# Optimization experiments

Measured on AMD Instinct MI355X. Metric: run time of the kernel, lower is better.

The kernel has to match this reference:

```python
import jax, jax.numpy as jnp
import numpy as np

N, E = 100000, 400000
ATOM_DIM, HIDDEN, LAYERS, HEADS = 74, 256, 3, 4
OUT = HIDDEN // HEADS


def setup_inputs() -> dict:
    key = jax.random.key(0)
    ks = jax.random.split(key, 12)
    s = 1.0 / np.sqrt(HIDDEN)
    return {
        'atom_feat': jax.random.normal(ks[0], (N, ATOM_DIM), jnp.float32),
        'src': jax.random.randint(ks[1], (E,), 0, N, jnp.int32),
        'dst': jax.random.randint(ks[2], (E,), 0, N, jnp.int32),
        'W_in': jax.random.normal(ks[3], (ATOM_DIM, HIDDEN), jnp.float32) / np.sqrt(ATOM_DIM),
        'b_in': jnp.zeros((HIDDEN,), jnp.float32),
        'W_src': jax.random.normal(ks[4], (LAYERS, HIDDEN, HIDDEN), jnp.float32) * s,
        'b_src': jnp.zeros((LAYERS, HIDDEN), jnp.float32),
        'W_dst': jax.random.normal(ks[5], (LAYERS, HIDDEN, HIDDEN), jnp.float32) * s,
        'b_dst': jnp.zeros((LAYERS, HIDDEN), jnp.float32),
        'attn': jax.random.normal(ks[6], (LAYERS, HEADS, OUT), jnp.float32) * s,
        'bias': jnp.zeros((LAYERS, HIDDEN), jnp.float32),
    }


def _gatv2_layer(h, src, dst, Ws, bs, Wd, bd, a, b_out):
    # h: [N, HIDDEN]; fc_src / fc_dst projections reshaped to [N, HEADS, OUT]
    fs = (h @ Ws + bs).reshape(N, HEADS, OUT)
    fd = (h @ Wd + bd).reshape(N, HEADS, OUT)
    # GATv2: e_ij = a . leaky_relu(Ws h_i + Wd h_j) per head  -> [E, HEADS]
    e = jax.nn.leaky_relu(fs[src] + fd[dst], negative_slope=0.2)
    logits = jnp.einsum('ehd,hd->eh', e, a)
    # segment softmax over incoming edges of each dst node
    m = jax.ops.segment_max(logits, dst, num_segments=N)      # [N, HEADS]
    ex = jnp.exp(logits - m[dst])
    denom = jax.ops.segment_sum(ex, dst, num_segments=N)      # [N, HEADS]
    alpha = ex / denom[dst]                                   # [E, HEADS]
    # weighted scatter-aggregate of source features -> [N, HEADS, OUT]
    msg = alpha[:, :, None] * fs[src]
    rst = jax.ops.segment_sum(msg, dst, num_segments=N)
    # flatten(1) + per-layer output bias
    return rst.reshape(N, HIDDEN) + b_out


def reference(atom_feat, src, dst, W_in, b_in, W_src, b_src, W_dst, b_dst, attn, bias):
    h = atom_feat @ W_in + b_in
    for l in range(LAYERS):
        h = _gatv2_layer(h, src, dst, W_src[l], b_src[l], W_dst[l], b_dst[l], attn[l], bias[l])
    return h  # [N, HIDDEN]; per-molecule list is just slicing of this matrix
```

## Files before the change

### kernel.cpp

```cpp
#include <hip/hip_runtime.h>
#include <hip/hip_fp16.h>

#define HID   256
#define NHEAD 4
#define DOUT  64
#define ADIM  74
#define KPAD_IN 96
#define LAYERS 3

typedef _Float16 half8 __attribute__((ext_vector_type(8)));
typedef _Float16 half4 __attribute__((ext_vector_type(4)));
typedef _Float16 half2v __attribute__((ext_vector_type(2)));
typedef float f32x4 __attribute__((ext_vector_type(4)));

__device__ __forceinline__ void gload16(const void* g, void* l) {
  __builtin_amdgcn_global_load_lds((const __attribute__((address_space(1))) void*)g,
                                   (__attribute__((address_space(3))) void*)l, 16, 0, 0);
}

__global__ void k_prep(const float* __restrict__ Ws, const float* __restrict__ Wd,
                       const float* __restrict__ Win,
                       _Float16* __restrict__ WT, _Float16* __restrict__ WTin) {
  int l = blockIdx.y;
  int id = blockIdx.x * 256 + threadIdx.x;
  if (l < LAYERS) {
    if (id >= 512 * HID) return;
    int n = id >> 8, k = id & 255;
    const float* W = (n < HID) ? (Ws + (size_t)l * HID * HID)
                               : (Wd + (size_t)l * HID * HID);
    int nn = (n < HID) ? n : (n - HID);
    WT[(size_t)l * 512 * HID + id] = (_Float16)W[k * HID + nn];
  } else {
    if (id >= HID * KPAD_IN) return;
    int n = id / KPAD_IN, k = id % KPAD_IN;
    WTin[id] = (_Float16)((k < ADIM) ? Win[k * HID + n] : 0.f);
  }
}

__device__ __forceinline__ void gemm_epilogue2(
    f32x4 acc[4][4], char* smem, int t, int lane, int wm, int wn,
    int row0, int col0, int M,
    const float* bias0, const float* bias1,
    _Float16* outS, _Float16* outD)
{
  const float* bp = (col0 < HID) ? (bias0 + col0) : (bias1 + (col0 - HID));
  _Float16*    op = (col0 < HID) ? (outS + col0) : (outD + (col0 - HID));
  _Float16 (*C)[136] = (_Float16(*)[136])smem;
  #pragma unroll
  for (int half = 0; half < 2; ++half) {
    __syncthreads();
    if (wm == half) {
      #pragma unroll
      for (int i = 0; i < 4; ++i) {
        #pragma unroll
        for (int j = 0; j < 4; ++j) {
          int lc = wn * 64 + j * 16 + (lane & 15);
          float bv = bp[lc];
          #pragma unroll
          for (int r = 0; r < 4; ++r) {
            int lr = i * 16 + (lane >> 4) * 4 + r;
            C[lr][lc] = (_Float16)(acc[i][j][r] + bv);
          }
        }
      }
    }
    __syncthreads();
    int lr = t >> 2, seg = t & 3;
    int grow = row0 + half * 64 + lr;
    if (grow < M) {
      const _Float16* sp = &C[lr][seg * 32];
      _Float16* dp = op + (size_t)grow * HID + seg * 32;
      #pragma unroll
      for (int q = 0; q < 4; ++q)
        *(uint4*)(dp + q * 8) = *(const uint4*)(sp + q * 8);
    }
  }
}

__global__ __launch_bounds__(256, 4)
void k_gemm_h(const _Float16* __restrict__ A, int M,
              const _Float16* __restrict__ B,
              const float* __restrict__ bias0, const float* __restrict__ bias1,
              _Float16* __restrict__ outS, _Float16* __restrict__ outD)
{
  __shared__ __align__(16) char smem[32768];
  const int t = threadIdx.x, lane = t & 63, wid = t >> 6;
  const int wm = wid >> 1, wn = wid & 1;
  const int nwg = gridDim.x, id = blockIdx.x;
  const int qc = nwg >> 3, rc = nwg & 7, xcd = id & 7, idx = id >> 3;
  const int swz = (xcd < rc ? xcd * (qc + 1) : rc * (qc + 1) + (xcd - rc) * qc) + idx;
  const int col0 = (swz & 3) * 128, row0 = (swz >> 2) * 128;

  f32x4 acc[4][4];
  #pragma unroll
  for (int i = 0; i < 4; ++i)
    #pragma unroll
    for (int j = 0; j < 4; ++j)
      acc[i][j] = (f32x4){0.f, 0.f, 0.f, 0.f};

  auto stage = [&](int kt, int buf) {
    const int kb = kt * 32;
    char* Ab = smem + buf * 16384;
    char* Bb = Ab + 8192;
    #pragma unroll
    for (int q = 0; q < 2; ++q) {
      int ci = wid * 2 + q;
      int lr = lane >> 2;
      int r = ci * 16 + lr;
      int slot = (lane & 3) ^ ((lr >> 1) & 3);
      int grow = row0 + r; grow = grow < M ? grow : (M - 1);
      gload16(A + (size_t)grow * HID + kb + slot * 8, Ab + ci * 1024);
      gload16(B + (size_t)(col0 + r) * HID + kb + slot * 8, Bb + ci * 1024);
    }
  };

  stage(0, 0);
  const int slot_off = (((lane >> 4) ^ ((lane >> 1) & 3)) << 4);
  const int ar0 = (wm * 64 + (lane & 15)) * 64 + slot_off;
  const int br0 = (wn * 64 + (lane & 15)) * 64 + slot_off;

  #pragma unroll
  for (int kt = 0; kt < 8; ++kt) {
    if (kt < 7) stage(kt + 1, (kt + 1) & 1);
    if (kt < 7) asm volatile("s_waitcnt vmcnt(4)" ::: "memory");
    else        asm volatile("s_waitcnt vmcnt(0)" ::: "memory");
    __builtin_amdgcn_s_barrier();
    __builtin_amdgcn_sched_barrier(0);
    const char* Ab = smem + (kt & 1) * 16384;
    const char* Bb = Ab + 8192;
    half8 af[4], bf[4];
    #pragma unroll
    for (int i = 0; i < 4; ++i) af[i] = *(const half8*)(Ab + ar0 + i * 1024);
    #pragma unroll
    for (int j = 0; j < 4; ++j) bf[j] = *(const half8*)(Bb + br0 + j * 1024);
    __builtin_amdgcn_s_setprio(1);
    #pragma unroll
    for (int i = 0; i < 4; ++i)
      #pragma unroll
      for (int j = 0; j < 4; ++j)
        acc[i][j] = __builtin_amdgcn_mfma_f32_16x16x32_f16(af[i], bf[j], acc[i][j], 0, 0, 0);
    __builtin_amdgcn_s_setprio(0);
    asm volatile("s_waitcnt lgkmcnt(0)" ::: "memory");
    __builtin_amdgcn_sched_barrier(0);
    __builtin_amdgcn_s_barrier();
    __builtin_amdgcn_sched_barrier(0);
  }
  gemm_epilogue2(acc, smem, t, lane, wm, wn, row0, col0, M, bias0, bias1, outS, outD);
}

__global__ __launch_bounds__(256)
void k_gemm_f(const float* __restrict__ A, int M,
              const _Float16* __restrict__ B,
              const float* __restrict__ bias0,
              _Float16* __restrict__ outS)
{
  __shared__ __align__(16) char smem[17408];
  const int t = threadIdx.x, lane = t & 63, wid = t >> 6;
  const int wm = wid >> 1, wn = wid & 1;
  const int nwg = gridDim.x, id = blockIdx.x;
  const int qc = nwg >> 3, rc = nwg & 7, xcd = id & 7, idx = id >> 3;
  const int swz = (xcd < rc ? xcd * (qc + 1) : rc * (qc + 1) + (xcd - rc) * qc) + idx;
  const int col0 = (swz & 1) * 128, row0 = (swz >> 1) * 128;
  char* Ab = smem;
  char* Bb = smem + 8192;

  f32x4 acc[4][4];
  #pragma unroll
  for (int i = 0; i < 4; ++i)
    #pragma unroll
    for (int j = 0; j < 4; ++j)
      acc[i][j] = (f32x4){0.f, 0.f, 0.f, 0.f};

  const int slot_off = (((lane >> 4) ^ ((lane >> 1) & 3)) << 4);
  const int ar0 = (wm * 64 + (lane & 15)) * 64 + slot_off;
  const int br0 = (wn * 64 + (lane & 15)) * 64 + slot_off;

  for (int kt = 0; kt < 3; ++kt) {
    const int kb = kt * 32;
    #pragma unroll
    for (int it = 0; it < 4; ++it) {
      int idx2 = t + it * 256;
      int r = idx2 >> 3, c4 = idx2 & 7;
      int gr = row0 + r;
      int k0 = kb + c4 * 4;
      float x0 = 0.f, x1 = 0.f, x2 = 0.f, x3 = 0.f;
      if (gr < M) {
        const float* ap = A + (size_t)gr * ADIM;
        if (k0 + 0 < ADIM) x0 = ap[k0 + 0];
        if (k0 + 1 < ADIM) x1 = ap[k0 + 1];
        if (k0 + 2 < ADIM) x2 = ap[k0 + 2];
        if (k0 + 3 < ADIM) x3 = ap[k0 + 3];
      }
      half4 hv = {(_Float16)x0, (_Float16)x1, (_Float16)x2, (_Float16)x3};
      int off = r * 64 + ((((c4 >> 1) ^ ((r >> 1) & 3)) << 4)) + (c4 & 1) * 8;
      *(half4*)(Ab + off) = hv;
    }
    #pragma unroll
    for (int q = 0; q < 2; ++q) {
      int ci = wid * 2 + q;
      int lr = lane >> 2;
      int r = ci * 16 + lr;
      int slot = (lane & 3) ^ ((lr >> 1) & 3);
      gload16(B + (size_t)(col0 + r) * KPAD_IN + kb + slot * 8, Bb + ci * 1024);
    }
    __syncthreads();
    half8 af[4], bf[4];
    #pragma unroll
    for (int i = 0; i < 4; ++i) af[i] = *(const half8*)(Ab + ar0 + i * 1024);
    #pragma unroll
    for (int j = 0; j < 4; ++j) bf[j] = *(const half8*)(Bb + br0 + j * 1024);
    #pragma unroll
    for (int i = 0; i < 4; ++i)
      #pragma unroll
      for (int j = 0; j < 4; ++j)
        acc[i][j] = __builtin_amdgcn_mfma_f32_16x16x32_f16(af[i], bf[j], acc[i][j], 0, 0, 0);
    __syncthreads();
  }
  gemm_epilogue2(acc, smem, t, lane, wm, wn, row0, col0, M, bias0, bias0, outS, outS);
}

__global__ __launch_bounds__(256)
void k_fused(const int* __restrict__ offs, const int* __restrict__ esrc,
             const int* __restrict__ perm,
             const _Float16* __restrict__ fs, const _Float16* __restrict__ fd,
             const float* __restrict__ attn, const float* __restrict__ bias,
             _Float16* __restrict__ hhalf, float* __restrict__ hfloat, int N)
{
  int gid = blockIdx.x * 8 + (threadIdx.x >> 5);
  if (gid >= N) return;
  int n = perm[gid];
  int sub = threadIdx.x & 31;
  int h = sub >> 3;
  int j0 = sub * 8;
  half8 fdv = *(const half8*)&fd[(size_t)n * HID + j0];
  float4 av0 = *(const float4*)&attn[h * DOUT + (sub & 7) * 8];
  float4 av1 = *(const float4*)&attn[h * DOUT + (sub & 7) * 8 + 4];
  float4 bv0 = *(const float4*)&bias[j0];
  float4 bv1 = *(const float4*)&bias[j0 + 4];
  half2v avh[4];
  avh[0] = (half2v){(_Float16)av0.x, (_Float16)av0.y};
  avh[1] = (half2v){(_Float16)av0.z, (_Float16)av0.w};
  avh[2] = (half2v){(_Float16)av1.x, (_Float16)av1.y};
  avh[3] = (half2v){(_Float16)av1.z, (_Float16)av1.w};
  half2v fd2[4];
  #pragma unroll
  for (int q = 0; q < 4; ++q) fd2[q] = (half2v){fdv[2 * q], fdv[2 * q + 1]};
  const half2v c02 = {(_Float16)0.2f, (_Float16)0.2f};
  float bvf[8] = {bv0.x, bv0.y, bv0.z, bv0.w, bv1.x, bv1.y, bv1.z, bv1.w};

  int t0 = offs[n], t1 = offs[n + 1];
  float m = -1e30f, ssum = 0.f;
  float a[8];
  #pragma unroll
  for (int q = 0; q < 8; ++q) a[q] = 0.f;

  half8 fE[4];
  #pragma unroll
  for (int k = 0; k < 4; ++k) {
    fE[k] = (half8){};
    if (t0 + k < t1) fE[k] = *(const half8*)&fs[(size_t)esrc[t0 + k] * HID + j0];
  }

  for (int tt = t0; tt < t1; tt += 4) {
    half8 fc[4];
    #pragma unroll
    for (int k = 0; k < 4; ++k) fc[k] = fE[k];
    #pragma unroll
    for (int k = 0; k < 4; ++k) {
      fE[k] = (half8){};
      if (tt + 4 + k < t1) fE[k] = *(const half8*)&fs[(size_t)esrc[tt + 4 + k] * HID + j0];
    }
    float p[4];
    #pragma unroll
    for (int k = 0; k < 4; ++k) {
      float acc = 0.f;
      #pragma unroll
      for (int q = 0; q < 4; ++q) {
        half2v xf = {fc[k][2 * q], fc[k][2 * q + 1]};
        half2v x = xf + fd2[q];
        half2v l = __builtin_elementwise_max(x, x * c02);
        acc = __builtin_amdgcn_fdot2(l, avh[q], acc, false);
      }
      p[k] = (tt + k < t1) ? acc : -1e30f;
    }
    #pragma unroll
    for (int k = 0; k < 4; ++k) {
      p[k] += __shfl_xor(p[k], 1);
      p[k] += __shfl_xor(p[k], 2);
      p[k] += __shfl_xor(p[k], 4);
    }
    float mx = fmaxf(fmaxf(fmaxf(p[0], p[1]), fmaxf(p[2], p[3])), m);
    float sc = __expf(m - mx);
    float w0 = __expf(p[0] - mx);
    float w1 = __expf(p[1] - mx);
    float w2 = __expf(p[2] - mx);
    float w3 = __expf(p[3] - mx);
    ssum = ssum * sc + w0 + w1 + w2 + w3;
    #pragma unroll
    for (int q = 0; q < 8; ++q) {
      float v = a[q] * sc;
      v += w0 * (float)fc[0][q];
      v += w1 * (float)fc[1][q];
      v += w2 * (float)fc[2][q];
      v += w3 * (float)fc[3][q];
      a[q] = v;
    }
    m = mx;
  }
  float inv = (t1 > t0) ? 1.0f / ssum : 0.f;
  float o[8];
  #pragma unroll
  for (int q = 0; q < 8; ++q) o[q] = a[q] * inv + bvf[q];
  if (hhalf) {
    half8 hv;
    #pragma unroll
    for (int q = 0; q < 8; ++q) hv[q] = (_Float16)o[q];
    *(half8*)&hhalf[(size_t)n * HID + j0] = hv;
  }
  if (hfloat) {
    float4 v0 = {o[0], o[1], o[2], o[3]};
    float4 v1 = {o[4], o[5], o[6], o[7]};
    *(float4*)&hfloat[(size_t)n * HID + j0] = v0;
    *(float4*)&hfloat[(size_t)n * HID + j0 + 4] = v1;
  }
}

__global__ void k_count(const int* __restrict__ dst, int* __restrict__ counts, int E) {
  int i = blockIdx.x * 256 + threadIdx.x;
  if (i < E) atomicAdd(&counts[dst[i]], 1);
}
__global__ __launch_bounds__(1024)
void k_scan1(const int* __restrict__ counts, int* __restrict__ offs,
             int* __restrict__ bsums, int* __restrict__ dhist, int N)
{
  __shared__ int sd[1024];
  __shared__ int hh[64];
  int t = threadIdx.x, i = blockIdx.x * 1024 + t;
  if (t < 64) hh[t] = 0;
  int x = (i < N) ? counts[i] : 0;
  sd[t] = x;
  __syncthreads();
  if (i < N) atomicAdd(&hh[x < 63 ? x : 63], 1);
  for (int off = 1; off < 1024; off <<= 1) {
    int v = (t >= off) ? sd[t - off] : 0;
    __syncthreads();
    sd[t] += v;
    __syncthreads();
  }
  if (i < N) offs[i] = sd[t] - x;
  if (t == 0) bsums[blockIdx.x] = sd[1023];
  __syncthreads();
  if (t < 64 && hh[t] > 0) atomicAdd(&dhist[t], hh[t]);
}
__global__ void k_scan2(const int* __restrict__ bsums, int* __restrict__ boffs,
                        int* __restrict__ offs, int nb, int N,
                        const int* __restrict__ dhist, int* __restrict__ dcur)
{
  int t = threadIdx.x;
  int x = dhist[t];
  int sum = x;
  for (int off = 1; off < 64; off <<= 1) {
    int v = __shfl_up(sum, off);
    if (t >= off) sum += v;
  }
  dcur[t] = sum - x;
  if (t == 0) {
    int run = 0;
    for (int b = 0; b < nb; ++b) { boffs[b] = run; run += bsums[b]; }
    offs[N] = run;
  }
}
__global__ __launch_bounds__(1024)
void k_scan3(const int* __restrict__ boffs, int* __restrict__ offs,
             int* __restrict__ cursor, int N)
{
  int i = blockIdx.x * 1024 + threadIdx.x;
  if (i < N) {
    int v = offs[i] + boffs[blockIdx.x];
    offs[i] = v;
    cursor[i] = v;
  }
}
__global__ void k_scatter(const int* __restrict__ src, const int* __restrict__ dst,
                          int* __restrict__ cursor, int* __restrict__ esrc, int E)
{
  int i = blockIdx.x * 256 + threadIdx.x;
  if (i < E) {
    int pos = atomicAdd(&cursor[dst[i]], 1);
    esrc[pos] = src[i];
  }
}
__global__ __launch_bounds__(256)
void k_deg_scatter(const int* __restrict__ counts, int* __restrict__ dcur,
                   int* __restrict__ perm, int N)
{
  __shared__ int hist[64];
  __shared__ int base[64];
  int t = threadIdx.x;
  int i = blockIdx.x * 256 + t;
  if (t < 64) hist[t] = 0;
  __syncthreads();
  int d = 0, lrank = 0;
  if (i < N) {
    d = counts[i]; d = d < 63 ? d : 63;
    lrank = atomicAdd(&hist[d], 1);
  }
  __syncthreads();
  if (t < 64 && hist[t] > 0) base[t] = atomicAdd(&dcur[t], hist[t]);
  __syncthreads();
  if (i < N) perm[base[d] + lrank] = i;
}

extern "C" void kernel_launch(void* const* d_in, const int* in_sizes, int n_in,
                              void* d_out, int out_size, void* d_ws, size_t ws_size,
                              hipStream_t stream)
{
  const float* atom  = (const float*)d_in[0];
  const int*   src   = (const int*)d_in[1];
  const int*   dst   = (const int*)d_in[2];
  const float* W_in  = (const float*)d_in[3];
  const float* b_in  = (const float*)d_in[4];
  const float* W_src = (const float*)d_in[5];
  const float* b_src = (const float*)d_in[6];
  const float* W_dst = (const float*)d_in[7];
  const float* b_dst = (const float*)d_in[8];
  const float* attn  = (const float*)d_in[9];
  const float* bias  = (const float*)d_in[10];

  const int N = in_sizes[0] / ADIM;
  const int E = in_sizes[1];
  _Float16* h_half = (_Float16*)d_out;
  float*    h_out  = (float*)d_out;

  char* w = (char*)d_ws;
  size_t off = 0;
  auto carve = [&](size_t bytes) {
    void* p = w + off;
    off = (off + bytes + 255) & ~(size_t)255;
    return p;
  };
  _Float16* fs    = (_Float16*)carve((size_t)N * HID * 2);
  _Float16* fd    = (_Float16*)carve((size_t)N * HID * 2);
  _Float16* WT    = (_Float16*)carve((size_t)LAYERS * 512 * HID * 2);
  _Float16* WTin  = (_Float16*)carve((size_t)HID * KPAD_IN * 2);
  int*      counts= (int*)carve((size_t)(N + 64) * 4);
  int*      offs  = (int*)carve((size_t)(N + 1) * 4);
  int*      cursor= (int*)carve((size_t)N * 4);
  int*      esrc  = (int*)carve((size_t)E * 4);
  int*      perm  = (int*)carve((size_t)N * 4);
  int*      dcur  = (int*)carve((size_t)64 * 4);
  int*      bsums = (int*)carve((size_t)1024 * 4);
  int*      boffs = (int*)carve((size_t)1024 * 4);
  int*      dhist = counts + N;
  (void)ws_size; (void)n_in; (void)out_size;

  const int nb = (N + 1023) / 1024;
  const int gmx = (N + 127) / 128;

  hipMemsetAsync(counts, 0, (size_t)(N + 64) * 4, stream);
  k_count<<<(E + 255) / 256, 256, 0, stream>>>(dst, counts, E);
  k_scan1<<<nb, 1024, 0, stream>>>(counts, offs, bsums, dhist, N);
  k_scan2<<<1, 64, 0, stream>>>(bsums, boffs, offs, nb, N, dhist, dcur);
  k_scan3<<<nb, 1024, 0, stream>>>(boffs, offs, cursor, N);
  k_scatter<<<(E + 255) / 256, 256, 0, stream>>>(src, dst, cursor, esrc, E);
  k_deg_scatter<<<(N + 255) / 256, 256, 0, stream>>>(counts, dcur, perm, N);

  k_prep<<<dim3(512, LAYERS + 1), 256, 0, stream>>>(W_src, W_dst, W_in, WT, WTin);
  k_gemm_f<<<2 * gmx, 256, 0, stream>>>(atom, N, WTin, b_in, h_half);

  for (int l = 0; l < LAYERS; ++l) {
    k_gemm_h<<<4 * gmx, 256, 0, stream>>>(h_half, N, WT + (size_t)l * 512 * HID,
                                          b_src + (size_t)l * HID,
                                          b_dst + (size_t)l * HID, fs, fd);
    const bool last = (l == LAYERS - 1);
    k_fused<<<(N + 7) / 8, 256, 0, stream>>>(offs, esrc, perm, fs, fd,
                                             attn + (size_t)l * NHEAD * DOUT,
                                             bias + (size_t)l * HID,
                                             last ? nullptr : h_half,
                                             last ? h_out : nullptr, N);
  }
}
```

Baseline: 458.4 us.

## Process two destination nodes per 32-lane group with interleaved edge loops

```diff
diff --git a/kernel.cpp b/kernel.cpp
--- a/kernel.cpp
+++ b/kernel.cpp
@@ -10,7 +10,6 @@
 
 typedef _Float16 half8 __attribute__((ext_vector_type(8)));
 typedef _Float16 half4 __attribute__((ext_vector_type(4)));
-typedef _Float16 half2v __attribute__((ext_vector_type(2)));
 typedef float f32x4 __attribute__((ext_vector_type(4)));
 
 __device__ __forceinline__ void gload16(const void* g, void* l) {
@@ -226,102 +225,132 @@
              const float* __restrict__ attn, const float* __restrict__ bias,
              _Float16* __restrict__ hhalf, float* __restrict__ hfloat, int N)
 {
-  int gid = blockIdx.x * 8 + (threadIdx.x >> 5);
-  if (gid >= N) return;
-  int n = perm[gid];
+  int grp = blockIdx.x * 8 + (threadIdx.x >> 5);
+  int g0 = grp * 2;
+  if (g0 >= N) return;
+  const bool has1 = (g0 + 1) < N;
+  int n0 = perm[g0];
+  int n1 = has1 ? perm[g0 + 1] : n0;
   int sub = threadIdx.x & 31;
   int h = sub >> 3;
   int j0 = sub * 8;
-  half8 fdv = *(const half8*)&fd[(size_t)n * HID + j0];
+
   float4 av0 = *(const float4*)&attn[h * DOUT + (sub & 7) * 8];
   float4 av1 = *(const float4*)&attn[h * DOUT + (sub & 7) * 8 + 4];
   float4 bv0 = *(const float4*)&bias[j0];
   float4 bv1 = *(const float4*)&bias[j0 + 4];
-  half2v avh[4];
-  avh[0] = (half2v){(_Float16)av0.x, (_Float16)av0.y};
-  avh[1] = (half2v){(_Float16)av0.z, (_Float16)av0.w};
-  avh[2] = (half2v){(_Float16)av1.x, (_Float16)av1.y};
-  avh[3] = (half2v){(_Float16)av1.z, (_Float16)av1.w};
-  half2v fd2[4];
-  #pragma unroll
-  for (int q = 0; q < 4; ++q) fd2[q] = (half2v){fdv[2 * q], fdv[2 * q + 1]};
-  const half2v c02 = {(_Float16)0.2f, (_Float16)0.2f};
+  float avf[8] = {av0.x, av0.y, av0.z, av0.w, av1.x, av1.y, av1.z, av1.w};
   float bvf[8] = {bv0.x, bv0.y, bv0.z, bv0.w, bv1.x, bv1.y, bv1.z, bv1.w};
 
-  int t0 = offs[n], t1 = offs[n + 1];
-  float m = -1e30f, ssum = 0.f;
-  float a[8];
-  #pragma unroll
-  for (int q = 0; q < 8; ++q) a[q] = 0.f;
-
-  half8 fE[4];
-  #pragma unroll
-  for (int k = 0; k < 4; ++k) {
-    fE[k] = (half8){};
-    if (t0 + k < t1) fE[k] = *(const half8*)&fs[(size_t)esrc[t0 + k] * HID + j0];
-  }
-
-  for (int tt = t0; tt < t1; tt += 4) {
-    half8 fc[4];
-    #pragma unroll
-    for (int k = 0; k < 4; ++k) fc[k] = fE[k];
-    #pragma unroll
-    for (int k = 0; k < 4; ++k) {
-      fE[k] = (half8){};
-      if (tt + 4 + k < t1) fE[k] = *(const half8*)&fs[(size_t)esrc[tt + 4 + k] * HID + j0];
-    }
-    float p[4];
-    #pragma unroll
-    for (int k = 0; k < 4; ++k) {
-      float acc = 0.f;
-      #pragma unroll
-      for (int q = 0; q < 4; ++q) {
-        half2v xf = {fc[k][2 * q], fc[k][2 * q + 1]};
-        half2v x = xf + fd2[q];
-        half2v l = __builtin_elementwise_max(x, x * c02);
-        acc = __builtin_amdgcn_fdot2(l, avh[q], acc, false);
-      }
-      p[k] = (tt + k < t1) ? acc : -1e30f;
-    }
-    #pragma unroll
-    for (int k = 0; k < 4; ++k) {
-      p[k] += __shfl_xor(p[k], 1);
-      p[k] += __shfl_xor(p[k], 2);
-      p[k] += __shfl_xor(p[k], 4);
-    }
-    float mx = fmaxf(fmaxf(fmaxf(p[0], p[1]), fmaxf(p[2], p[3])), m);
-    float sc = __expf(m - mx);
-    float w0 = __expf(p[0] - mx);
-    float w1 = __expf(p[1] - mx);
-    float w2 = __expf(p[2] - mx);
-    float w3 = __expf(p[3] - mx);
-    ssum = ssum * sc + w0 + w1 + w2 + w3;
+  half8 fdh0 = *(const half8*)&fd[(size_t)n0 * HID + j0];
+  half8 fdh1 = *(const half8*)&fd[(size_t)n1 * HID + j0];
+  float fd0[8], fd1[8];
+  #pragma unroll
+  for (int q = 0; q < 8; ++q) { fd0[q] = (float)fdh0[q]; fd1[q] = (float)fdh1[q]; }
+
+  int t00 = offs[n0], t01 = offs[n0 + 1];
+  int t10 = has1 ? offs[n1] : 0;
+  int t11 = has1 ? offs[n1 + 1] : 0;
+
+  float m0 = -1e30f, s0 = 0.f, m1 = -1e30f, s1 = 0.f;
+  float a0[8], a1[8];
+  #pragma unroll
+  for (int q = 0; q < 8; ++q) { a0[q] = 0.f; a1[q] = 0.f; }
+
+  half8 pA0 = {}, pB0 = {}, pA1 = {}, pB1 = {};
+  if (t00 < t01)     pA0 = *(const half8*)&fs[(size_t)esrc[t00] * HID + j0];
+  if (t00 + 1 < t01) pB0 = *(const half8*)&fs[(size_t)esrc[t00 + 1] * HID + j0];
+  if (t10 < t11)     pA1 = *(const half8*)&fs[(size_t)esrc[t10] * HID + j0];
+  if (t10 + 1 < t11) pB1 = *(const half8*)&fs[(size_t)esrc[t10 + 1] * HID + j0];
+
+  int tt0 = t00, tt1 = t10;
+  while (tt0 < t01 || tt1 < t11) {
+    const bool vA0 = tt0 < t01, vB0 = tt0 + 1 < t01;
+    const bool vA1 = tt1 < t11, vB1 = tt1 + 1 < t11;
+    half8 fA0 = pA0, fB0 = pB0, fA1 = pA1, fB1 = pB1;
+    pA0 = (half8){}; pB0 = (half8){}; pA1 = (half8){}; pB1 = (half8){};
+    if (tt0 + 2 < t01) pA0 = *(const half8*)&fs[(size_t)esrc[tt0 + 2] * HID + j0];
+    if (tt0 + 3 < t01) pB0 = *(const half8*)&fs[(size_t)esrc[tt0 + 3] * HID + j0];
+    if (tt1 + 2 < t11) pA1 = *(const half8*)&fs[(size_t)esrc[tt1 + 2] * HID + j0];
+    if (tt1 + 3 < t11) pB1 = *(const half8*)&fs[(size_t)esrc[tt1 + 3] * HID + j0];
+
+    float fa0[8], fb0[8], fa1[8], fb1[8];
     #pragma unroll
     for (int q = 0; q < 8; ++q) {
-      float v = a[q] * sc;
-      v += w0 * (float)fc[0][q];
-      v += w1 * (float)fc[1][q];
-      v += w2 * (float)fc[2][q];
-      v += w3 * (float)fc[3][q];
-      a[q] = v;
-    }
-    m = mx;
-  }
-  float inv = (t1 > t0) ? 1.0f / ssum : 0.f;
-  float o[8];
-  #pragma unroll
-  for (int q = 0; q < 8; ++q) o[q] = a[q] * inv + bvf[q];
+      fa0[q] = (float)fA0[q]; fb0[q] = (float)fB0[q];
+      fa1[q] = (float)fA1[q]; fb1[q] = (float)fB1[q];
+    }
+    float qa0 = 0.f, qb0 = 0.f, qa1 = 0.f, qb1 = 0.f;
+    #pragma unroll
+    for (int q = 0; q < 8; ++q) {
+      float x;
+      x = fa0[q] + fd0[q]; x = x > 0.f ? x : 0.2f * x; qa0 += x * avf[q];
+      x = fb0[q] + fd0[q]; x = x > 0.f ? x : 0.2f * x; qb0 += x * avf[q];
+      x = fa1[q] + fd1[q]; x = x > 0.f ? x : 0.2f * x; qa1 += x * avf[q];
+      x = fb1[q] + fd1[q]; x = x > 0.f ? x : 0.2f * x; qb1 += x * avf[q];
+    }
+    qa0 += __shfl_xor(qa0, 1); qb0 += __shfl_xor(qb0, 1);
+    qa1 += __shfl_xor(qa1, 1); qb1 += __shfl_xor(qb1, 1);
+    qa0 += __shfl_xor(qa0, 2); qb0 += __shfl_xor(qb0, 2);
+    qa1 += __shfl_xor(qa1, 2); qb1 += __shfl_xor(qb1, 2);
+    qa0 += __shfl_xor(qa0, 4); qb0 += __shfl_xor(qb0, 4);
+    qa1 += __shfl_xor(qa1, 4); qb1 += __shfl_xor(qb1, 4);
+    qa0 = vA0 ? qa0 : -1e30f;
+    qb0 = vB0 ? qb0 : -1e30f;
+    qa1 = vA1 ? qa1 : -1e30f;
+    qb1 = vB1 ? qb1 : -1e30f;
+    float mx0 = fmaxf(fmaxf(qa0, qb0), m0);
+    float sc0 = __expf(m0 - mx0);
+    float wa0 = __expf(qa0 - mx0);
+    float wb0 = __expf(qb0 - mx0);
+    float mx1 = fmaxf(fmaxf(qa1, qb1), m1);
+    float sc1 = __expf(m1 - mx1);
+    float wa1 = __expf(qa1 - mx1);
+    float wb1 = __expf(qb1 - mx1);
+    s0 = s0 * sc0 + wa0 + wb0;
+    s1 = s1 * sc1 + wa1 + wb1;
+    #pragma unroll
+    for (int q = 0; q < 8; ++q) {
+      a0[q] = a0[q] * sc0 + wa0 * fa0[q] + wb0 * fb0[q];
+      a1[q] = a1[q] * sc1 + wa1 * fa1[q] + wb1 * fb1[q];
+    }
+    m0 = mx0; m1 = mx1;
+    tt0 += 2; tt1 += 2;
+  }
+
+  float inv0 = (t01 > t00) ? 1.0f / s0 : 0.f;
+  float o0[8];
+  #pragma unroll
+  for (int q = 0; q < 8; ++q) o0[q] = a0[q] * inv0 + bvf[q];
   if (hhalf) {
     half8 hv;
     #pragma unroll
-    for (int q = 0; q < 8; ++q) hv[q] = (_Float16)o[q];
-    *(half8*)&hhalf[(size_t)n * HID + j0] = hv;
+    for (int q = 0; q < 8; ++q) hv[q] = (_Float16)o0[q];
+    *(half8*)&hhalf[(size_t)n0 * HID + j0] = hv;
   }
   if (hfloat) {
-    float4 v0 = {o[0], o[1], o[2], o[3]};
-    float4 v1 = {o[4], o[5], o[6], o[7]};
-    *(float4*)&hfloat[(size_t)n * HID + j0] = v0;
-    *(float4*)&hfloat[(size_t)n * HID + j0 + 4] = v1;
+    float4 v0 = {o0[0], o0[1], o0[2], o0[3]};
+    float4 v1 = {o0[4], o0[5], o0[6], o0[7]};
+    *(float4*)&hfloat[(size_t)n0 * HID + j0] = v0;
+    *(float4*)&hfloat[(size_t)n0 * HID + j0 + 4] = v1;
+  }
+  if (has1) {
+    float inv1 = (t11 > t10) ? 1.0f / s1 : 0.f;
+    float o1[8];
+    #pragma unroll
+    for (int q = 0; q < 8; ++q) o1[q] = a1[q] * inv1 + bvf[q];
+    if (hhalf) {
+      half8 hv;
+      #pragma unroll
+      for (int q = 0; q < 8; ++q) hv[q] = (_Float16)o1[q];
+      *(half8*)&hhalf[(size_t)n1 * HID + j0] = hv;
+    }
+    if (hfloat) {
+      float4 v0 = {o1[0], o1[1], o1[2], o1[3]};
+      float4 v1 = {o1[4], o1[5], o1[6], o1[7]};
+      *(float4*)&hfloat[(size_t)n1 * HID + j0] = v0;
+      *(float4*)&hfloat[(size_t)n1 * HID + j0 + 4] = v1;
+    }
   }
 }
 
@@ -473,10 +502,10 @@
                                           b_src + (size_t)l * HID,
                                           b_dst + (size_t)l * HID, fs, fd);
     const bool last = (l == LAYERS - 1);
-    k_fused<<<(N + 7) / 8, 256, 0, stream>>>(offs, esrc, perm, fs, fd,
-                                             attn + (size_t)l * NHEAD * DOUT,
-                                             bias + (size_t)l * HID,
-                                             last ? nullptr : h_half,
-                                             last ? h_out : nullptr, N);
-  }
-}
+    k_fused<<<(N + 15) / 16, 256, 0, stream>>>(offs, esrc, perm, fs, fd,
+                                               attn + (size_t)l * NHEAD * DOUT,
+                                               bias + (size_t)l * HID,
+                                               last ? nullptr : h_half,
+                                               last ? h_out : nullptr, N);
+  }
+}
```

New measurement: 471.2 us. +2.8%, slower.
